# Kernel optimization log

Hardware: AMD Instinct MI355X
Metric: run time of the kernel (lower is better)

Reference implementation:

```python
import jax, jax.numpy as jnp
import numpy as np

V = 100000   # char_size
E = 256      # embedding_dim
H = 512      # hidden_dim
Hh = H // 2  # per-direction hidden
L = 20       # label_size
T = 4096     # sequence length
START = 18
STOP = 19
NEG = -10000.0


def setup_inputs() -> dict:
    key = jax.random.key(0)
    ks = jax.random.split(key, 16)
    s = 0.05
    x = jax.random.randint(ks[0], (1, T), 0, V, dtype=jnp.int32)
    emb = jax.random.normal(ks[1], (V, E), jnp.float32) * s
    w_ih_f = jax.random.normal(ks[2], (4 * Hh, E), jnp.float32) * s
    w_hh_f = jax.random.normal(ks[3], (4 * Hh, Hh), jnp.float32) * s
    b_ih_f = jax.random.normal(ks[4], (4 * Hh,), jnp.float32) * s
    b_hh_f = jax.random.normal(ks[5], (4 * Hh,), jnp.float32) * s
    w_ih_b = jax.random.normal(ks[6], (4 * Hh, E), jnp.float32) * s
    w_hh_b = jax.random.normal(ks[7], (4 * Hh, Hh), jnp.float32) * s
    b_ih_b = jax.random.normal(ks[8], (4 * Hh,), jnp.float32) * s
    b_hh_b = jax.random.normal(ks[9], (4 * Hh,), jnp.float32) * s
    w_out = jax.random.normal(ks[10], (L, H), jnp.float32) * s
    b_out = jax.random.normal(ks[11], (L,), jnp.float32) * s
    transitions = jax.random.normal(ks[12], (L, L), jnp.float32)
    transitions = transitions.at[START, :].set(NEG).at[:, STOP].set(NEG)
    h0 = jax.random.normal(ks[13], (2, Hh), jnp.float32)  # [direction, Hh], batch=1
    c0 = jax.random.normal(ks[14], (2, Hh), jnp.float32)
    return {"x": x, "emb": emb,
            "w_ih_f": w_ih_f, "w_hh_f": w_hh_f, "b_ih_f": b_ih_f, "b_hh_f": b_hh_f,
            "w_ih_b": w_ih_b, "w_hh_b": w_hh_b, "b_ih_b": b_ih_b, "b_hh_b": b_hh_b,
            "w_out": w_out, "b_out": b_out, "transitions": transitions,
            "h0": h0, "c0": c0}


def _lstm_dir(xs, w_ih, w_hh, b_ih, b_hh, h0, c0, reverse):
    # xs: [T, E]; PyTorch gate order i, f, g, o
    def step(carry, x_t):
        h, c = carry
        z = x_t @ w_ih.T + b_ih + h @ w_hh.T + b_hh  # [4*Hh]
        i, f, g, o = jnp.split(z, 4)
        i = jax.nn.sigmoid(i); f = jax.nn.sigmoid(f); o = jax.nn.sigmoid(o)
        g = jnp.tanh(g)
        c = f * c + i * g
        h = o * jnp.tanh(c)
        return (h, c), h
    _, hs = jax.lax.scan(step, (h0, c0), xs, reverse=reverse)
    return hs  # [T, Hh]


def _viterbi(feats, transitions):
    # feats: [T, L]; transitions[to, from]
    alpha0 = jnp.full((L,), NEG, feats.dtype).at[START].set(0.0)
    trT = transitions.T  # [from, to]
    def step(alpha, frame):
        smat = alpha[:, None] + frame[None, :] + trT  # [from, to]
        return jnp.max(smat, axis=0), jnp.argmax(smat, axis=0)
    alpha, bptrs = jax.lax.scan(step, alpha0, feats)  # bptrs: [T, L]
    final = alpha + transitions[STOP, :]
    score = jnp.max(final)
    best_last = jnp.argmax(final)
    def back(tag, bp):
        prev = bp[tag]
        return prev, prev
    _, prevs = jax.lax.scan(back, best_last, bptrs[1:], reverse=True)  # [T-1]
    path = jnp.concatenate([prevs, best_last[None]])  # [T]
    return score, path


def reference(x, emb, w_ih_f, w_hh_f, b_ih_f, b_hh_f, w_ih_b, w_hh_b, b_ih_b, b_hh_b,
              w_out, b_out, transitions, h0, c0):
    xs = emb[x[0]]  # [T, E], batch = 1
    h_f = _lstm_dir(xs, w_ih_f, w_hh_f, b_ih_f, b_hh_f, h0[0], c0[0], reverse=False)
    h_b = _lstm_dir(xs, w_ih_b, w_hh_b, b_ih_b, b_hh_b, h0[1], c0[1], reverse=True)
    lstm_out = jnp.concatenate([h_f, h_b], axis=-1)  # [T, H]
    feats = lstm_out @ w_out.T + b_out  # [T, L]
    score, path = _viterbi(feats, transitions)
    return score, path
```

## Files before the change

kernel.cpp:

```cpp
#include <hip/hip_runtime.h>
#include <hip/hip_bf16.h>
#include <stdint.h>

#define TT 4096
#define EE 256
#define LL 20
#define STARTT 18
#define STOPP 19
#define NEGV -10000.0f
#define NCH 256

typedef short v8s __attribute__((ext_vector_type(8)));
typedef float v4f __attribute__((ext_vector_type(4)));
typedef int   v4i __attribute__((ext_vector_type(4)));

__device__ inline float bf2f(unsigned short u){
  unsigned int x = ((unsigned int)u) << 16;
  return __builtin_bit_cast(float, x);
}
__device__ inline unsigned short f2bf(float f){
  unsigned int x = __builtin_bit_cast(unsigned int, f);
  unsigned int r = (x + 0x7FFFu + ((x >> 16) & 1u)) >> 16;
  return (unsigned short)r;
}

#define BARRIER_LDS() asm volatile("s_waitcnt lgkmcnt(0)\ns_barrier" ::: "memory")

constexpr size_t OFF_U    = 0;
constexpr size_t SZ_U     = 2ull*TT*1024*2;
constexpr size_t OFF_X    = OFF_U + SZ_U;
constexpr size_t SZ_X     = (size_t)TT*EE*2;
constexpr size_t OFF_WIH  = OFF_X + SZ_X;
constexpr size_t SZ_WIH   = 2048ull*256*2;
constexpr size_t OFF_BIAS = OFF_WIH + SZ_WIH;
constexpr size_t SZ_BIAS  = 2048ull*4;
constexpr size_t OFF_WQ   = OFF_BIAS + SZ_BIAS;
constexpr size_t SZ_WQ    = 2ull*8*8*4*64*16;
constexpr size_t OFF_FS   = OFF_WQ + SZ_WQ;
constexpr size_t SZ_FS    = 2ull*256*16;
constexpr size_t OFF_WOP  = OFF_FS + SZ_FS;
constexpr size_t SZ_WOP   = 32ull*512*2;
constexpr size_t OFF_HOUT = OFF_WOP + SZ_WOP;
constexpr size_t SZ_HOUT  = (size_t)TT*512*2;
constexpr size_t OFF_FE   = OFF_HOUT + SZ_HOUT;
constexpr size_t SZ_FE    = (size_t)TT*LL*4;
constexpr size_t OFF_P    = OFF_FE + SZ_FE;
constexpr size_t SZ_P     = 256ull*400*4;
constexpr size_t OFF_BAL  = OFF_P + SZ_P;
constexpr size_t SZ_BAL   = 20736;
constexpr size_t OFF_BP   = OFF_BAL + SZ_BAL;
constexpr size_t SZ_BP    = (size_t)TT*LL;
constexpr size_t OFF_M    = OFF_BP + SZ_BP;
constexpr size_t SZ_M     = 256ull*LL;
constexpr size_t OFF_EG   = OFF_M + SZ_M + 64;


__global__ void k_gather(const int* __restrict__ x, const float* __restrict__ emb,
                         unsigned short* __restrict__ X){
  int t = blockIdx.x;
  int xt = x[t];
  const float4* src = (const float4*)(emb + (size_t)xt * EE);
  float4 v = src[threadIdx.x];
  ushort4 o;
  o.x = f2bf(v.x); o.y = f2bf(v.y); o.z = f2bf(v.z); o.w = f2bf(v.w);
  ((ushort4*)(X + (size_t)t * EE))[threadIdx.x] = o;
}

__global__ void k_wih(const float* __restrict__ wf, const float* __restrict__ wb,
                      unsigned short* __restrict__ WIH){
  int gid = blockIdx.x * 256 + threadIdx.x;
  int row = gid >> 5, c8 = gid & 31;
  const float* src = (row < 1024 ? wf + (size_t)row * EE : wb + (size_t)(row - 1024) * EE) + c8 * 8;
  unsigned short* dst = WIH + (size_t)row * 256 + c8 * 8;
#pragma unroll
  for (int i = 0; i < 8; i++) dst[i] = f2bf(src[i]);
}

__global__ void k_bias(const float* bf, const float* hf, const float* bb, const float* hb,
                       float* __restrict__ bias){
  int i = blockIdx.x * 256 + threadIdx.x;
  int r = i & 1023;
  bias[i] = (i < 1024) ? (bf[r] + hf[r]) : (bb[r] + hb[r]);
}

__global__ void k_wout(const float* __restrict__ wout, unsigned short* __restrict__ WOP){
  int gid = blockIdx.x * 256 + threadIdx.x;
  int row = gid >> 9, k = gid & 511;
  WOP[gid] = (row < LL) ? f2bf(wout[row * 512 + k]) : 0;
}

__global__ void k_whh8(const float* __restrict__ whf, const float* __restrict__ whb,
                       unsigned int* __restrict__ WQ, float* __restrict__ FS){
  int row = blockIdx.x;
  int d = row >> 10, R = row & 1023;
  int g = R >> 8, J = R & 255;
  int w = J >> 5, tp = (J >> 4) & 1, n = J & 15;
  int nt = g * 2 + tp;
  const float* W = (d ? whb : whf) + (size_t)R * 256;
  int t = threadIdx.x;
  float4 v = ((const float4*)W)[t];
  float m = fmaxf(fmaxf(fabsf(v.x), fabsf(v.y)), fmaxf(fabsf(v.z), fabsf(v.w)));
#pragma unroll
  for (int o = 32; o >= 1; o >>= 1) m = fmaxf(m, __shfl_down(m, o));
  m = __shfl(m, 0);
  float sc = (m > 0.f) ? (m / 127.f) : 1.f;
  float inv = 1.f / sc;
  int a = (int)rintf(v.x * inv), b = (int)rintf(v.y * inv);
  int c = (int)rintf(v.z * inv), e4 = (int)rintf(v.w * inv);
  unsigned int pack = ((unsigned)a & 255u) | (((unsigned)b & 255u) << 8)
                    | (((unsigned)c & 255u) << 16) | (((unsigned)e4 & 255u) << 24);
  int kt = t >> 4, q = (t >> 2) & 3, comp = t & 3;
  int lane = q * 16 + n;
  size_t widx = ((((size_t)d * 8 + w) * 8 + nt) * 4 + kt) * 64 + lane;
  WQ[widx * 4 + comp] = pack;
  if (t == 0) FS[((size_t)d * 256 + J) * 4 + g] = sc;
}

__global__ void k_gemm_u(const unsigned short* __restrict__ X,
                         const unsigned short* __restrict__ WIH,
                         const float* __restrict__ bias,
                         unsigned short* __restrict__ U){
  int wave = threadIdx.x >> 6, l = threadIdx.x & 63;
  int tile = blockIdx.x * 4 + wave;
  int mt = tile & 255, nt = tile >> 8;
  int lm = l & 15, lq = l >> 4;
  const unsigned short* Arow = X   + (size_t)(mt * 16 + lm) * 256 + lq * 8;
  const unsigned short* Brow = WIH + (size_t)(nt * 16 + lm) * 256 + lq * 8;
  v4f acc = {0.f, 0.f, 0.f, 0.f};
#pragma unroll
  for (int kb = 0; kb < 8; kb++){
    v8s a = *(const v8s*)(Arow + kb * 32);
    v8s b = *(const v8s*)(Brow + kb * 32);
    acc = __builtin_amdgcn_mfma_f32_16x16x32_bf16(a, b, acc, 0, 0, 0);
  }
  int n = nt * 16 + lm;
  int dd = n >> 10, r = n & 1023;
  int g = r >> 8, J = r & 255;
  float bi = bias[n];
#pragma unroll
  for (int r4 = 0; r4 < 4; r4++){
    int t = mt * 16 + lq * 4 + r4;
    U[(((size_t)(dd * TT + t)) * 256 + J) * 4 + g] = f2bf(acc[r4] + bi);
  }
}


#define NT8(M) M(0) M(1) M(2) M(3) M(4) M(5) M(6) M(7)

#define DECLWB(nt) v4i wb0_##nt, wb1_##nt, wb2_##nt, wb3_##nt;
#define LOADWB(nt) { wb0_##nt = WQv[base + ((nt)*4 + 0) * 64]; \
                     wb1_##nt = WQv[base + ((nt)*4 + 1) * 64]; \
                     wb2_##nt = WQv[base + ((nt)*4 + 2) * 64]; \
                     wb3_##nt = WQv[base + ((nt)*4 + 3) * 64]; }
#define DECLACC(nt) v4i acc_##nt;
#define MFA(nt) acc_##nt = __builtin_amdgcn_mfma_i32_16x16x64_i8(hA0, wb0_##nt, zero,     0, 0, 0);
#define MFB(nt) acc_##nt = __builtin_amdgcn_mfma_i32_16x16x64_i8(hA1, wb1_##nt, acc_##nt, 0, 0, 0);
#define MFC(nt) acc_##nt = __builtin_amdgcn_mfma_i32_16x16x64_i8(hA2, wb2_##nt, acc_##nt, 0, 0, 0);
#define MFD(nt) acc_##nt = __builtin_amdgcn_mfma_i32_16x16x64_i8(hA3, wb3_##nt, acc_##nt, 0, 0, 0);

__global__ void __launch_bounds__(512)
__attribute__((amdgpu_waves_per_eu(2, 2)))
k_lstm12(
    const unsigned short* __restrict__ U, const v4i* __restrict__ WQv,
    const float4* __restrict__ FS4, const float* __restrict__ h0,
    const float* __restrict__ c0, unsigned short* __restrict__ hout){
  int d = blockIdx.x;
  int tid = threadIdx.x;
  int w = tid >> 6;
  int l = tid & 63;
  int q = l >> 4;
  int n = l & 15;
  int tp = l >> 5;
  int Jsel = w * 32 + tp * 16 + n;
  bool pub = ((l & 16) == 0);

  __shared__ __align__(16) unsigned char hb[2][256];

  NT8(DECLWB)
  {
    size_t base = ((size_t)(d * 8 + w)) * 2048 + l;
    NT8(LOADWB)
  }

  float4 fsv = FS4[(size_t)d * 256 + Jsel];
  float fs8x = fsv.x * (8.f/127.f), fs1x = fsv.x * (1.f/127.f);
  float fs8y = fsv.y * (8.f/127.f), fs1y = fsv.y * (1.f/127.f);
  float fs8z = fsv.z * (8.f/127.f), fs1z = fsv.z * (1.f/127.f);
  float fs8w = fsv.w * (8.f/127.f), fs1w = fsv.w * (1.f/127.f);

  float cst = c0[d * 256 + Jsel];
  if (pub){
    float hini = h0[d * 256 + Jsel];
    hini = fminf(fmaxf(hini, -8.f), 8.f);
    hb[0][Jsel] = (unsigned char)(char)(int)rintf(hini * (127.f / 8.f));
  }

  const unsigned short* Up0 = U + (size_t)d * TT * 1024 + (size_t)Jsel * 4;
  int stp = d ? -1 : 1;
  int tA = d ? TT - 1 : 0;
  uint2 u_c = *(const uint2*)(Up0 + (size_t)tA * 1024);
  uint2 u_n = *(const uint2*)(Up0 + (size_t)(tA + stp) * 1024);

  unsigned short* hp = hout + (size_t)tA * 512 + d * 256 + Jsel;

  v4i zero = {0, 0, 0, 0};

  __syncthreads();

  for (int s = 0; s < TT; s++){
    int par = s & 1;
    int tt = d ? (TT - 1 - s) : s;

    const char* hbase = (const char*)(&hb[par][0]) + (q << 4);
    v4i hA0 = *(const v4i*)(hbase);
    v4i hA1 = *(const v4i*)(hbase + 64);
    v4i hA2 = *(const v4i*)(hbase + 128);
    v4i hA3 = *(const v4i*)(hbase + 192);

    NT8(DECLACC)
    NT8(MFA)
    NT8(MFB)
    NT8(MFC)
    NT8(MFD)

    int aI = tp ? acc_1[0] : acc_0[0];
    int aF = tp ? acc_3[0] : acc_2[0];
    int aG = tp ? acc_5[0] : acc_4[0];
    int aO = tp ? acc_7[0] : acc_6[0];

    bool s0 = (s == 0);
    float fx = s0 ? fs8x : fs1x;
    float fy = s0 ? fs8y : fs1y;
    float fz = s0 ? fs8z : fs1z;
    float fw = s0 ? fs8w : fs1w;

    float u_i = bf2f((unsigned short)(u_c.x & 0xffffu));
    float u_f = bf2f((unsigned short)(u_c.x >> 16));
    float u_g = bf2f((unsigned short)(u_c.y & 0xffffu));
    float u_o = bf2f((unsigned short)(u_c.y >> 16));
    float zi = fmaf((float)aI, fx, u_i);
    float zf = fmaf((float)aF, fy, u_f);
    float zg = fmaf((float)aG, fz, u_g);
    float zo = fmaf((float)aO, fw, u_o);

    u_c = u_n;
    {
      int t2 = tt + 2 * stp;
      t2 = t2 < 0 ? 0 : (t2 > TT - 1 ? TT - 1 : t2);
      u_n = *(const uint2*)(Up0 + (size_t)t2 * 1024);
    }

    float za = fminf(fmaxf(zi, -87.f), 87.f);
    float ea = __expf(-za);
    float gi = __builtin_amdgcn_rcpf(1.f + ea);
    float zb = fminf(fmaxf(zf, -87.f), 87.f);
    float eb = __expf(-zb);
    float gf = __builtin_amdgcn_rcpf(1.f + eb);
    float zc = fminf(fmaxf(zg, -20.f), 20.f);
    float ec = __expf(-2.f * zc);
    float gg = (1.f - ec) * __builtin_amdgcn_rcpf(1.f + ec);
    float zd = fminf(fmaxf(zo, -87.f), 87.f);
    float ed = __expf(-zd);
    float go = __builtin_amdgcn_rcpf(1.f + ed);

    cst = fmaf(gf, cst, gi * gg);
    float cc = fminf(fmaxf(cst, -20.f), 20.f);
    float e2 = __expf(-2.f * cc);
    float th = (1.f - e2) * __builtin_amdgcn_rcpf(1.f + e2);
    float h = go * th;

    if (pub){
      int qv = (int)rintf(fminf(fmaxf(h, -1.f), 1.f) * 127.f);
      hb[par ^ 1][Jsel] = (unsigned char)(char)qv;
      *hp = f2bf(h);
    }
    hp += stp * 512;

    BARRIER_LDS();
  }
}

__global__ void k_feats2(const unsigned short* __restrict__ HOUT,
                         const unsigned short* __restrict__ WOP,
                         const float* __restrict__ bout,
                         float* __restrict__ feats){
  int wave = threadIdx.x >> 6, l = threadIdx.x & 63;
  int tile = blockIdx.x * 4 + wave;
  int mt = tile & 255, nt = tile >> 8;
  int lm = l & 15, lq = l >> 4;
  const unsigned short* Arow = HOUT + (size_t)(mt * 16 + lm) * 512 + lq * 8;
  const unsigned short* Brow = WOP  + (size_t)(nt * 16 + lm) * 512 + lq * 8;
  v4f acc = {0.f, 0.f, 0.f, 0.f};
#pragma unroll
  for (int kb = 0; kb < 16; kb++){
    v8s a = *(const v8s*)(Arow + kb * 32);
    v8s b = *(const v8s*)(Brow + kb * 32);
    acc = __builtin_amdgcn_mfma_f32_16x16x32_bf16(a, b, acc, 0, 0, 0);
  }
  int n = nt * 16 + lm;
  if (n < LL){
    float bi = bout[n];
#pragma unroll
    for (int r4 = 0; r4 < 4; r4++){
      int t = mt * 16 + lq * 4 + r4;
      feats[t * LL + n] = acc[r4] + bi;
    }
  }
}

__global__ void k_vchunk(const float* __restrict__ feats, const float* __restrict__ trans,
                         float* __restrict__ P){
  int c = blockIdx.x, j = threadIdx.x;
  __shared__ float Ps[2][LL][LL];
  bool act = j < LL;
  float trow[LL];
  if (act){
#pragma unroll
    for (int i = 0; i < LL; i++) trow[i] = trans[j * LL + i];
    for (int i = 0; i < LL; i++) Ps[0][i][j] = (i == j) ? 0.f : -1e30f;
  }
  __syncthreads();
  for (int s = 0; s < 16; s++){
    int t = c * 16 + s;
    int pb = s & 1;
    if (act){
      float fj = feats[t * LL + j];
      for (int i = 0; i < LL; i++){
        float m = Ps[pb][i][0] + trow[0];
#pragma unroll
        for (int mm = 1; mm < LL; mm++) m = fmaxf(m, Ps[pb][i][mm] + trow[mm]);
        Ps[pb ^ 1][i][j] = m + fj;
      }
    }
    __syncthreads();
  }
  if (act)
    for (int i = 0; i < LL; i++) P[((size_t)c * LL + i) * LL + j] = Ps[0][i][j];
}

__global__ void k_vscan(const float* __restrict__ P, float* __restrict__ bal){
  int tid = threadIdx.x;
  bool act = tid < LL;
  __shared__ float al[LL];
  __shared__ float Pl[400];
  if (act){
    float a = (tid == STARTT) ? 0.f : NEGV;
    al[tid] = a;
    bal[tid] = a;
  }
  for (int k = tid; k < 400; k += 64) Pl[k] = P[k];
  __syncthreads();
  for (int c = 0; c < NCH; c++){
    float p0 = 0.f, p1 = 0.f, p2 = 0.f, p3 = 0.f, p4 = 0.f, p5 = 0.f, p6 = 0.f;
    if (c + 1 < NCH){
      const float* Pn = P + (size_t)(c + 1) * 400;
      p0 = Pn[tid];        p1 = Pn[tid + 64];  p2 = Pn[tid + 128];
      p3 = Pn[tid + 192];  p4 = Pn[tid + 256]; p5 = Pn[tid + 320];
      if (tid + 384 < 400) p6 = Pn[tid + 384];
    }
    float m = -1e30f;
    if (act){
      m = al[0] + Pl[tid];
#pragma unroll
      for (int i = 1; i < LL; i++) m = fmaxf(m, al[i] + Pl[i * LL + tid]);
    }
    __syncthreads();
    if (act){
      al[tid] = m;
      bal[(c + 1) * LL + tid] = m;
    }
    if (c + 1 < NCH){
      Pl[tid] = p0;        Pl[tid + 64] = p1;  Pl[tid + 128] = p2;
      Pl[tid + 192] = p3;  Pl[tid + 256] = p4; Pl[tid + 320] = p5;
      if (tid + 384 < 400) Pl[tid + 384] = p6;
    }
    __syncthreads();
  }
}

__global__ void k_vbp(const float* __restrict__ feats, const float* __restrict__ trans,
                      const float* __restrict__ bal, unsigned char* __restrict__ bp,
                      unsigned char* __restrict__ M){
  int c = blockIdx.x, j = threadIdx.x;
  bool act = j < LL;
  __shared__ float al[2][LL];
  __shared__ unsigned char bpl[16][LL];
  float trow[LL];
  if (act){
#pragma unroll
    for (int i = 0; i < LL; i++) trow[i] = trans[j * LL + i];
    al[0][j] = bal[c * LL + j];
  }
  __syncthreads();
  for (int s = 0; s < 16; s++){
    int t = c * 16 + s;
    int pb = s & 1;
    if (act){
      float m = al[pb][0] + trow[0];
      int arg = 0;
#pragma unroll
      for (int i = 1; i < LL; i++){
        float v = al[pb][i] + trow[i];
        if (v > m){ m = v; arg = i; }
      }
      bpl[s][j] = (unsigned char)arg;
      bp[(size_t)t * LL + j] = (unsigned char)arg;
      al[pb ^ 1][j] = m + feats[t * LL + j];
    }
    __syncthreads();
  }
  if (act){
    int tag = j;
    for (int s = 15; s >= 0; s--) tag = bpl[s][tag];
    M[c * LL + j] = (unsigned char)tag;
  }
}

__global__ void k_vtag(const float* __restrict__ bal, const float* __restrict__ trans,
                       const unsigned char* __restrict__ M, int* __restrict__ Eg,
                       float* __restrict__ out){
  int tid = threadIdx.x;
  __shared__ unsigned char Ml[NCH * LL];
  __shared__ float fin[LL];
  for (int k = tid; k < NCH * LL; k += 64) Ml[k] = M[k];
  if (tid < LL) fin[tid] = bal[NCH * LL + tid] + trans[STOPP * LL + tid];
  __syncthreads();
  if (tid == 0){
    float m = fin[0]; int arg = 0;
    for (int i = 1; i < LL; i++) if (fin[i] > m){ m = fin[i]; arg = i; }
    out[0] = m;
    int tag = arg;
    Eg[NCH - 1] = tag;
    for (int c = NCH - 1; c >= 1; c--){
      tag = Ml[c * LL + tag];
      Eg[c - 1] = tag;
    }
  }
}

__global__ void k_vemit(const int* __restrict__ Eg, const unsigned char* __restrict__ bp,
                        float* __restrict__ out){
  int c = threadIdx.x;
  int tag = Eg[c];
  out[1 + c * 16 + 15] = (float)tag;
  for (int s = 15; s >= 1; s--){
    tag = bp[(size_t)(c * 16 + s) * LL + tag];
    out[1 + c * 16 + s - 1] = (float)tag;
  }
}

extern "C" void kernel_launch(void* const* d_in, const int* in_sizes, int n_in,
                              void* d_out, int out_size, void* d_ws, size_t ws_size,
                              hipStream_t stream){
  (void)in_sizes; (void)n_in; (void)out_size; (void)ws_size;
  const int*   x     = (const int*)d_in[0];
  const float* emb   = (const float*)d_in[1];
  const float* wihf  = (const float*)d_in[2];
  const float* whhf  = (const float*)d_in[3];
  const float* bihf  = (const float*)d_in[4];
  const float* bhhf  = (const float*)d_in[5];
  const float* wihb  = (const float*)d_in[6];
  const float* whhb  = (const float*)d_in[7];
  const float* bihb  = (const float*)d_in[8];
  const float* bhhb  = (const float*)d_in[9];
  const float* wout  = (const float*)d_in[10];
  const float* bout  = (const float*)d_in[11];
  const float* trans = (const float*)d_in[12];
  const float* h0    = (const float*)d_in[13];
  const float* c0    = (const float*)d_in[14];
  float* out = (float*)d_out;
  char* ws = (char*)d_ws;

  unsigned short* U    = (unsigned short*)(ws + OFF_U);
  unsigned short* X    = (unsigned short*)(ws + OFF_X);
  unsigned short* WIH  = (unsigned short*)(ws + OFF_WIH);
  float*          BIAS = (float*)(ws + OFF_BIAS);
  unsigned int*   WQ   = (unsigned int*)(ws + OFF_WQ);
  float*          FS   = (float*)(ws + OFF_FS);
  unsigned short* WOP  = (unsigned short*)(ws + OFF_WOP);
  unsigned short* HOUT = (unsigned short*)(ws + OFF_HOUT);
  float*          FE   = (float*)(ws + OFF_FE);
  float*          P    = (float*)(ws + OFF_P);
  float*          BAL  = (float*)(ws + OFF_BAL);
  unsigned char*  BP   = (unsigned char*)(ws + OFF_BP);
  unsigned char*  M    = (unsigned char*)(ws + OFF_M);
  int*            EG   = (int*)(ws + OFF_EG);

  k_gather<<<TT, 64, 0, stream>>>(x, emb, X);
  k_wih<<<256, 256, 0, stream>>>(wihf, wihb, WIH);
  k_bias<<<8, 256, 0, stream>>>(bihf, bhhf, bihb, bhhb, BIAS);
  k_wout<<<64, 256, 0, stream>>>(wout, WOP);
  k_whh8<<<2048, 64, 0, stream>>>(whhf, whhb, WQ, FS);
  k_gemm_u<<<8192, 256, 0, stream>>>(X, WIH, BIAS, U);
  k_lstm12<<<2, 512, 0, stream>>>(U, (const v4i*)WQ, (const float4*)FS, h0, c0, HOUT);
  k_feats2<<<128, 256, 0, stream>>>(HOUT, WOP, bout, FE);
  k_vchunk<<<NCH, 64, 0, stream>>>(FE, trans, P);
  k_vscan<<<1, 64, 0, stream>>>(P, BAL);
  k_vbp<<<NCH, 64, 0, stream>>>(FE, trans, BAL, BP, M);
  k_vtag<<<1, 64, 0, stream>>>(BAL, trans, M, EG, out);
  k_vemit<<<1, 256, 0, stream>>>(EG, BP, out);
}
```

Before: 3.199 ms.

## Offload one gate tile to sdot4 and interleave MFMA with gate activations

Moves the eighth weight tile (output-gate tile for one half of the lanes) out of the MFMA chain and computes it with packed int8 dot products on the VALU plus a cross-lane shuffle reduction. It also interleaves the gate nonlinearities with the MFMA groups so activation math overlaps matrix work on the serial recurrence critical path. Several clamps are dropped from the sigmoid inputs and the h quantization. This adds VALU work, shuffles and a new weight layout, and removing the clamps risks overflow or wraparound in int8 quantization if values go out of range.

```diff
diff --git a/kernel.cpp b/kernel.cpp
--- a/kernel.cpp
+++ b/kernel.cpp
@@ -23,6 +23,18 @@
   unsigned int r = (x + 0x7FFFu + ((x >> 16) & 1u)) >> 16;
   return (unsigned short)r;
 }
+
+#if __has_builtin(__builtin_amdgcn_sdot4)
+#define SDOT4(a,b,c) __builtin_amdgcn_sdot4((int)(a),(int)(b),(c),false)
+#else
+__device__ inline int sdot4_sw(int a, int b, int c){
+  return c + (int)(char)(a)        * (int)(char)(b)
+           + (int)(char)(a >> 8)   * (int)(char)(b >> 8)
+           + (int)(char)(a >> 16)  * (int)(char)(b >> 16)
+           + (int)(char)(a >> 24)  * (int)(char)(b >> 24);
+}
+#define SDOT4(a,b,c) sdot4_sw((int)(a),(int)(b),(c))
+#endif
 
 #define BARRIER_LDS() asm volatile("s_waitcnt lgkmcnt(0)\ns_barrier" ::: "memory")
 
@@ -36,7 +48,9 @@
 constexpr size_t SZ_BIAS  = 2048ull*4;
 constexpr size_t OFF_WQ   = OFF_BIAS + SZ_BIAS;
 constexpr size_t SZ_WQ    = 2ull*8*8*4*64*16;
-constexpr size_t OFF_FS   = OFF_WQ + SZ_WQ;
+constexpr size_t OFF_WQD  = OFF_WQ + SZ_WQ;
+constexpr size_t SZ_WQD   = 2ull*8*4*64*16;
+constexpr size_t OFF_FS   = OFF_WQD + SZ_WQD;
 constexpr size_t SZ_FS    = 2ull*256*16;
 constexpr size_t OFF_WOP  = OFF_FS + SZ_FS;
 constexpr size_t SZ_WOP   = 32ull*512*2;
@@ -89,8 +103,9 @@
   WOP[gid] = (row < LL) ? f2bf(wout[row * 512 + k]) : 0;
 }
 
-__global__ void k_whh8(const float* __restrict__ whf, const float* __restrict__ whb,
-                       unsigned int* __restrict__ WQ, float* __restrict__ FS){
+__global__ void k_whh9(const float* __restrict__ whf, const float* __restrict__ whb,
+                       unsigned int* __restrict__ WQ, unsigned int* __restrict__ WQD,
+                       float* __restrict__ FS){
   int row = blockIdx.x;
   int d = row >> 10, R = row & 1023;
   int g = R >> 8, J = R & 255;
@@ -111,8 +126,13 @@
                     | (((unsigned)c & 255u) << 16) | (((unsigned)e4 & 255u) << 24);
   int kt = t >> 4, q = (t >> 2) & 3, comp = t & 3;
   int lane = q * 16 + n;
-  size_t widx = ((((size_t)d * 8 + w) * 8 + nt) * 4 + kt) * 64 + lane;
-  WQ[widx * 4 + comp] = pack;
+  if (nt == 7){
+    size_t didx = (((size_t)d * 8 + w) * 4 + kt) * 64 + lane;
+    WQD[didx * 4 + comp] = pack;
+  } else {
+    size_t widx = ((((size_t)d * 8 + w) * 8 + nt) * 4 + kt) * 64 + lane;
+    WQ[widx * 4 + comp] = pack;
+  }
   if (t == 0) FS[((size_t)d * 256 + J) * 4 + g] = sc;
 }
 
@@ -145,25 +165,26 @@
 }
 
 
-#define NT8(M) M(0) M(1) M(2) M(3) M(4) M(5) M(6) M(7)
+#define NT7(M) M(0) M(1) M(2) M(3) M(4) M(5) M(6)
 
 #define DECLWB(nt) v4i wb0_##nt, wb1_##nt, wb2_##nt, wb3_##nt;
 #define LOADWB(nt) { wb0_##nt = WQv[base + ((nt)*4 + 0) * 64]; \
                      wb1_##nt = WQv[base + ((nt)*4 + 1) * 64]; \
                      wb2_##nt = WQv[base + ((nt)*4 + 2) * 64]; \
                      wb3_##nt = WQv[base + ((nt)*4 + 3) * 64]; }
-#define DECLACC(nt) v4i acc_##nt;
-#define MFA(nt) acc_##nt = __builtin_amdgcn_mfma_i32_16x16x64_i8(hA0, wb0_##nt, zero,     0, 0, 0);
-#define MFB(nt) acc_##nt = __builtin_amdgcn_mfma_i32_16x16x64_i8(hA1, wb1_##nt, acc_##nt, 0, 0, 0);
-#define MFC(nt) acc_##nt = __builtin_amdgcn_mfma_i32_16x16x64_i8(hA2, wb2_##nt, acc_##nt, 0, 0, 0);
-#define MFD(nt) acc_##nt = __builtin_amdgcn_mfma_i32_16x16x64_i8(hA3, wb3_##nt, acc_##nt, 0, 0, 0);
+#define MF4(nt) \
+  acc_##nt = __builtin_amdgcn_mfma_i32_16x16x64_i8(hA0, wb0_##nt, zero,     0, 0, 0); \
+  acc_##nt = __builtin_amdgcn_mfma_i32_16x16x64_i8(hA1, wb1_##nt, acc_##nt, 0, 0, 0); \
+  acc_##nt = __builtin_amdgcn_mfma_i32_16x16x64_i8(hA2, wb2_##nt, acc_##nt, 0, 0, 0); \
+  acc_##nt = __builtin_amdgcn_mfma_i32_16x16x64_i8(hA3, wb3_##nt, acc_##nt, 0, 0, 0);
 
 __global__ void __launch_bounds__(512)
 __attribute__((amdgpu_waves_per_eu(2, 2)))
-k_lstm12(
+k_lstm13(
     const unsigned short* __restrict__ U, const v4i* __restrict__ WQv,
-    const float4* __restrict__ FS4, const float* __restrict__ h0,
-    const float* __restrict__ c0, unsigned short* __restrict__ hout){
+    const v4i* __restrict__ WQDv, const float4* __restrict__ FS4,
+    const float* __restrict__ h0, const float* __restrict__ c0,
+    unsigned short* __restrict__ hout){
   int d = blockIdx.x;
   int tid = threadIdx.x;
   int w = tid >> 6;
@@ -176,10 +197,14 @@
 
   __shared__ __align__(16) unsigned char hb[2][256];
 
-  NT8(DECLWB)
+  NT7(DECLWB)
+  v4i wd0, wd1, wd2, wd3;
   {
     size_t base = ((size_t)(d * 8 + w)) * 2048 + l;
-    NT8(LOADWB)
+    NT7(LOADWB)
+    size_t dbase = ((size_t)(d * 8 + w)) * 256 + l;
+    wd0 = WQDv[dbase];        wd1 = WQDv[dbase + 64];
+    wd2 = WQDv[dbase + 128];  wd3 = WQDv[dbase + 192];
   }
 
   float4 fsv = FS4[(size_t)d * 256 + Jsel];
@@ -217,31 +242,58 @@
     v4i hA2 = *(const v4i*)(hbase + 128);
     v4i hA3 = *(const v4i*)(hbase + 192);
 
-    NT8(DECLACC)
-    NT8(MFA)
-    NT8(MFB)
-    NT8(MFC)
-    NT8(MFD)
-
-    int aI = tp ? acc_1[0] : acc_0[0];
-    int aF = tp ? acc_3[0] : acc_2[0];
-    int aG = tp ? acc_5[0] : acc_4[0];
-    int aO = tp ? acc_7[0] : acc_6[0];
-
     bool s0 = (s == 0);
     float fx = s0 ? fs8x : fs1x;
     float fy = s0 ? fs8y : fs1y;
     float fz = s0 ? fs8z : fs1z;
     float fw = s0 ? fs8w : fs1w;
-
     float u_i = bf2f((unsigned short)(u_c.x & 0xffffu));
     float u_f = bf2f((unsigned short)(u_c.x >> 16));
     float u_g = bf2f((unsigned short)(u_c.y & 0xffffu));
     float u_o = bf2f((unsigned short)(u_c.y >> 16));
+
+    int ad = 0;
+    ad = SDOT4(wd0.x, hA0.x, ad); ad = SDOT4(wd0.y, hA0.y, ad);
+    ad = SDOT4(wd0.z, hA0.z, ad); ad = SDOT4(wd0.w, hA0.w, ad);
+    ad = SDOT4(wd1.x, hA1.x, ad); ad = SDOT4(wd1.y, hA1.y, ad);
+    ad = SDOT4(wd1.z, hA1.z, ad); ad = SDOT4(wd1.w, hA1.w, ad);
+    ad = SDOT4(wd2.x, hA2.x, ad); ad = SDOT4(wd2.y, hA2.y, ad);
+    ad = SDOT4(wd2.z, hA2.z, ad); ad = SDOT4(wd2.w, hA2.w, ad);
+    ad = SDOT4(wd3.x, hA3.x, ad); ad = SDOT4(wd3.y, hA3.y, ad);
+    ad = SDOT4(wd3.z, hA3.z, ad); ad = SDOT4(wd3.w, hA3.w, ad);
+    ad += __shfl_xor(ad, 16);
+    ad += __shfl_xor(ad, 32);
+
+    v4i acc_0, acc_1, acc_2, acc_3, acc_4, acc_5, acc_6;
+    MF4(0) MF4(1)
+    int aI = tp ? acc_1[0] : acc_0[0];
     float zi = fmaf((float)aI, fx, u_i);
+    float ea = __expf(-zi);
+    float gi = __builtin_amdgcn_rcpf(1.f + ea);
+
+    MF4(2) MF4(3)
+    int aF = tp ? acc_3[0] : acc_2[0];
     float zf = fmaf((float)aF, fy, u_f);
+    float eb = __expf(-zf);
+    float gf = __builtin_amdgcn_rcpf(1.f + eb);
+
+    MF4(4) MF4(5)
+    int aG = tp ? acc_5[0] : acc_4[0];
     float zg = fmaf((float)aG, fz, u_g);
+    float zc = fminf(fmaxf(zg, -20.f), 20.f);
+    float ec = __expf(-2.f * zc);
+    float gg = (1.f - ec) * __builtin_amdgcn_rcpf(1.f + ec);
+    cst = fmaf(gf, cst, gi * gg);
+    float cc = fminf(fmaxf(cst, -20.f), 20.f);
+    float e2 = __expf(-2.f * cc);
+    float th = (1.f - e2) * __builtin_amdgcn_rcpf(1.f + e2);
+
+    MF4(6)
+    int aO = tp ? ad : acc_6[0];
     float zo = fmaf((float)aO, fw, u_o);
+    float ed = __expf(-zo);
+    float go = __builtin_amdgcn_rcpf(1.f + ed);
+    float h = go * th;
 
     u_c = u_n;
     {
@@ -250,27 +302,8 @@
       u_n = *(const uint2*)(Up0 + (size_t)t2 * 1024);
     }
 
-    float za = fminf(fmaxf(zi, -87.f), 87.f);
-    float ea = __expf(-za);
-    float gi = __builtin_amdgcn_rcpf(1.f + ea);
-    float zb = fminf(fmaxf(zf, -87.f), 87.f);
-    float eb = __expf(-zb);
-    float gf = __builtin_amdgcn_rcpf(1.f + eb);
-    float zc = fminf(fmaxf(zg, -20.f), 20.f);
-    float ec = __expf(-2.f * zc);
-    float gg = (1.f - ec) * __builtin_amdgcn_rcpf(1.f + ec);
-    float zd = fminf(fmaxf(zo, -87.f), 87.f);
-    float ed = __expf(-zd);
-    float go = __builtin_amdgcn_rcpf(1.f + ed);
-
-    cst = fmaf(gf, cst, gi * gg);
-    float cc = fminf(fmaxf(cst, -20.f), 20.f);
-    float e2 = __expf(-2.f * cc);
-    float th = (1.f - e2) * __builtin_amdgcn_rcpf(1.f + e2);
-    float h = go * th;
-
     if (pub){
-      int qv = (int)rintf(fminf(fmaxf(h, -1.f), 1.f) * 127.f);
+      int qv = (int)rintf(h * 127.f);
       hb[par ^ 1][Jsel] = (unsigned char)(char)qv;
       *hp = f2bf(h);
     }
@@ -476,6 +509,7 @@
   unsigned short* WIH  = (unsigned short*)(ws + OFF_WIH);
   float*          BIAS = (float*)(ws + OFF_BIAS);
   unsigned int*   WQ   = (unsigned int*)(ws + OFF_WQ);
+  unsigned int*   WQD  = (unsigned int*)(ws + OFF_WQD);
   float*          FS   = (float*)(ws + OFF_FS);
   unsigned short* WOP  = (unsigned short*)(ws + OFF_WOP);
   unsigned short* HOUT = (unsigned short*)(ws + OFF_HOUT);
@@ -490,9 +524,10 @@
   k_wih<<<256, 256, 0, stream>>>(wihf, wihb, WIH);
   k_bias<<<8, 256, 0, stream>>>(bihf, bhhf, bihb, bhhb, BIAS);
   k_wout<<<64, 256, 0, stream>>>(wout, WOP);
-  k_whh8<<<2048, 64, 0, stream>>>(whhf, whhb, WQ, FS);
+  k_whh9<<<2048, 64, 0, stream>>>(whhf, whhb, WQ, WQD, FS);
   k_gemm_u<<<8192, 256, 0, stream>>>(X, WIH, BIAS, U);
-  k_lstm12<<<2, 512, 0, stream>>>(U, (const v4i*)WQ, (const float4*)FS, h0, c0, HOUT);
+  k_lstm13<<<2, 512, 0, stream>>>(U, (const v4i*)WQ, (const v4i*)WQD,
+                                  (const float4*)FS, h0, c0, HOUT);
   k_feats2<<<128, 256, 0, stream>>>(HOUT, WOP, bout, FE);
   k_vchunk<<<NCH, 64, 0, stream>>>(FE, trans, P);
   k_vscan<<<1, 64, 0, stream>>>(P, BAL);
```

New measurement: 3.758 ms. +17.5%, slower.
